# Kernel tuning notes

Measured on AMD Instinct MI355X. Metric: run time of the kernel, lower is better.

Reference implementation:

```python
import jax, jax.numpy as jnp
import numpy as np

B, L, E, H = 2, 2048, 1024, 16
HD = E // H


def _rel_shift(x):
    # x: [b, h, q, k] -> Transformer-XL relative shift via pad+reshape trick
    b, h, q, k = x.shape
    xp = jnp.pad(x, ((0, 0), (0, 0), (0, 0), (1, 0)))  # pad left of last dim
    xp = xp.reshape(b, h, k + 1, q)
    return xp[:, :, 1:, :].reshape(b, h, q, k)


def setup_inputs() -> dict:
    key = jax.random.key(0)
    ks = jax.random.split(key, 16)
    s = 0.02
    return {
        "query": jax.random.normal(ks[0], (B, L, E), jnp.float32),
        "key": jax.random.normal(ks[1], (B, L, E), jnp.float32),
        "value": jax.random.normal(ks[2], (B, L, E), jnp.float32),
        "pos_embedding": jax.random.normal(ks[3], (B, L, E), jnp.float32),
        "Wq": jax.random.normal(ks[4], (E, E), jnp.float32) * s,
        "bq": jnp.zeros((E,), jnp.float32),
        "Wk": jax.random.normal(ks[5], (E, E), jnp.float32) * s,
        "bk": jnp.zeros((E,), jnp.float32),
        "Wv": jax.random.normal(ks[6], (E, E), jnp.float32) * s,
        "bv": jnp.zeros((E,), jnp.float32),
        "Wp": jax.random.normal(ks[7], (E, E), jnp.float32) * s,  # Pos linear, no bias
        "Wo": jax.random.normal(ks[8], (E, E), jnp.float32) * s,
        "bo": jnp.zeros((E,), jnp.float32),
        "U": jax.random.normal(ks[9], (H, HD), jnp.float32) * s,
        "V": jax.random.normal(ks[10], (H, HD), jnp.float32) * s,
    }


def reference(query, key, value, pos_embedding, Wq, bq, Wk, bk, Wv, bv, Wp, Wo, bo, U, V):
    b, qlen, e = query.shape
    h, hd = U.shape
    scale = jnp.sqrt(jnp.asarray(e, query.dtype))
    # torch Linear: y = x @ W.T + b
    q = (query @ Wq.T + bq).reshape(b, qlen, h, hd)
    k = (key @ Wk.T + bk).reshape(b, key.shape[1], h, hd)
    v = (value @ Wv.T + bv).reshape(b, value.shape[1], h, hd)
    r = (pos_embedding @ Wp.T).reshape(b, -1, h, hd)
    content_score = jnp.einsum("bqhd,bkhd->bhqk", q + U, k)
    position_score = jnp.einsum("bqhd,bkhd->bhqk", q + V, r)
    position_score = _rel_shift(position_score)
    attention_score = (content_score + position_score) / scale
    # NOTE: the original module applies NO softmax; faithful reproduction.
    # einsum 'bhqk,bvhd->bqhd' sums over both k (scores) and v (values).
    alpha = jnp.einsum("bhqk,bvhd->bqhd", attention_score, v).reshape(b, qlen, e)
    return alpha @ Wo.T + bo
```

## Files before the change

### kernel.cpp

```cpp
#include <hip/hip_runtime.h>

#define BB 2
#define LL 2048
#define EE 1024
#define HH 16
#define HDD 64

typedef __bf16 bf16x8 __attribute__((ext_vector_type(8)));
typedef float f32x4 __attribute__((ext_vector_type(4)));

__device__ __forceinline__ unsigned short f2bf(float f) {
  unsigned int x = __float_as_uint(f);
  return (unsigned short)((x + 0x7FFFu + ((x >> 16) & 1u)) >> 16);
}

__device__ __forceinline__ float bf2f(unsigned short u) {
  return __uint_as_float((unsigned int)u << 16);
}

__device__ __forceinline__ void load_lds16(const void* g, void* l) {
  __builtin_amdgcn_global_load_lds(
      (const __attribute__((address_space(1))) void*)g,
      (__attribute__((address_space(3))) void*)l, 16, 0, 0);
}

#define SUMKV_BLOCKS 256
#define CAST_BLOCKS 1280
#define CAST_STRIDE (CAST_BLOCKS * 256)
__global__ __launch_bounds__(256) void prelude_kernel(
    const float* __restrict__ q, const float* __restrict__ pe,
    const float* __restrict__ wq, const float* __restrict__ wp,
    unsigned short* __restrict__ q16, unsigned short* __restrict__ pe16,
    unsigned short* __restrict__ wq16, unsigned short* __restrict__ wp16,
    const float* __restrict__ key, const float* __restrict__ value,
    float* __restrict__ keysum, float* __restrict__ valsum) {
  if (blockIdx.x < SUMKV_BLOCKS) {
    int blk2 = blockIdx.x;
    int b = blk2 >> 7, ch = blk2 & 127;
    int tid = threadIdx.x;
    const float4* k4 = (const float4*)(key   + ((size_t)b * LL + ch * 16) * EE);
    const float4* v4 = (const float4*)(value + ((size_t)b * LL + ch * 16) * EE);
    float4 ak = make_float4(0.f, 0.f, 0.f, 0.f);
    float4 av = make_float4(0.f, 0.f, 0.f, 0.f);
#pragma unroll 8
    for (int i = 0; i < 16; i++) {
      float4 kk = k4[i * 256 + tid];
      float4 vv = v4[i * 256 + tid];
      ak.x += kk.x; ak.y += kk.y; ak.z += kk.z; ak.w += kk.w;
      av.x += vv.x; av.y += vv.y; av.z += vv.z; av.w += vv.w;
    }
    int e = tid * 4;
    atomicAdd(&keysum[b * EE + e + 0], ak.x);
    atomicAdd(&keysum[b * EE + e + 1], ak.y);
    atomicAdd(&keysum[b * EE + e + 2], ak.z);
    atomicAdd(&keysum[b * EE + e + 3], ak.w);
    atomicAdd(&valsum[b * EE + e + 0], av.x);
    atomicAdd(&valsum[b * EE + e + 1], av.y);
    atomicAdd(&valsum[b * EE + e + 2], av.z);
    atomicAdd(&valsum[b * EE + e + 3], av.w);
  } else {
    const int NQ4 = BB * LL * EE / 4;
    const int NW4 = EE * EE / 4;
    int t = (blockIdx.x - SUMKV_BLOCKS) * 256 + threadIdx.x;
    float4 v[8]; unsigned short* dst[8]; int off[8];
#pragma unroll
    for (int k = 0; k < 8; k++) {
      int i = t + k * CAST_STRIDE;
      const float* src;
      if (i < NQ4)                { src = q;  dst[k] = q16;  off[k] = i; }
      else if (i < 2 * NQ4)       { src = pe; dst[k] = pe16; off[k] = i - NQ4; }
      else if (i < 2 * NQ4 + NW4) { src = wq; dst[k] = wq16; off[k] = i - 2 * NQ4; }
      else                        { src = wp; dst[k] = wp16; off[k] = i - 2 * NQ4 - NW4; }
      v[k] = ((const float4*)src)[off[k]];
    }
#pragma unroll
    for (int k = 0; k < 8; k++) {
      ushort4 u;
      u.x = f2bf(v[k].x); u.y = f2bf(v[k].y); u.z = f2bf(v[k].z); u.w = f2bf(v[k].w);
      ((ushort4*)dst[k])[off[k]] = u;
    }
  }
}

__global__ __launch_bounds__(256) void proj_kernel(
    const float* __restrict__ keysum, const float* __restrict__ valsum,
    const float* __restrict__ Wk, const float* __restrict__ bk,
    const float* __restrict__ Wv, const float* __restrict__ bv,
    float* __restrict__ Kproj, float* __restrict__ Vproj) {
  int wv = threadIdx.x >> 6, lane = threadIdx.x & 63;
  int idx = blockIdx.x * 4 + wv;
  int b = idx >> 10, ep = idx & (EE - 1);
  const float* sum  = blockIdx.z ? valsum : keysum;
  const float* W    = blockIdx.z ? Wv : Wk;
  const float* bias = blockIdx.z ? bv : bk;
  float* outp       = blockIdx.z ? Vproj : Kproj;
  float acc = 0.f;
  for (int k = lane; k < EE; k += 64) acc += sum[b * EE + k] * W[ep * EE + k];
  for (int off = 32; off; off >>= 1) acc += __shfl_down(acc, off, 64);
  if (lane == 0) outp[b * EE + ep] = acc + (float)LL * bias[ep];
}

__global__ __launch_bounds__(256) void gemm_kernel(
    const unsigned short* __restrict__ q16, const unsigned short* __restrict__ wq16,
    const float* __restrict__ bq, unsigned short* __restrict__ qout,
    const unsigned short* __restrict__ pe16, const unsigned short* __restrict__ wp16,
    unsigned short* __restrict__ rout, float* __restrict__ chunks,
    const float* __restrict__ Vproj, const float* __restrict__ Wo,
    float* __restrict__ W2) {
  const int tid = threadIdx.x;
  const int lane = tid & 63;
  const int wv = tid >> 6;

  if (blockIdx.z == 2) {
    int bid = blockIdx.x + 32 * blockIdx.y;
    int wslot = bid * 4 + wv;
    int base = wslot * 32;
    int b = base >> 14;
    int h = (base >> 10) & (HH - 1);
    int e0 = base & (EE - 1);
    float vp = Vproj[b * EE + h * HDD + lane];
    const float* wo = Wo + (size_t)e0 * EE + h * HDD + lane;
    for (int r = 0; r < 32; r++) {
      float acc = vp * wo[(size_t)r * EE];
      for (int off = 32; off; off >>= 1) acc += __shfl_down(acc, off, 64);
      if (lane == 0) W2[((size_t)b * HH + h) * EE + e0 + r] = acc;
    }
    return;
  }

  const int K = EE, N = EE;
  const unsigned short* X; const unsigned short* W; const float* bias;
  unsigned short* Out;
  if (blockIdx.z == 0) { X = q16;  W = wq16; bias = bq;      Out = qout; }
  else                 { X = pe16; W = wp16; bias = nullptr; Out = rout; }

  __shared__ __align__(16) unsigned short As[2][128 * 32];
  __shared__ __align__(16) unsigned short Bs[2][128 * 32];

  const int wr = wv >> 1, wc = wv & 1;
  const int m0 = blockIdx.x * 128;
  const int n0 = blockIdx.y * 128;

  const int srow = wv * 16 + (lane >> 2);
  const int s_src = ((lane & 3) - ((lane >> 3) & 3)) & 3;
  const unsigned short* gA = X + (size_t)(m0 + srow) * K + s_src * 8;
  const unsigned short* gB = W + (size_t)(n0 + srow) * K + s_src * 8;

  f32x4 acc[4][4];
#pragma unroll
  for (int i = 0; i < 4; i++)
#pragma unroll
    for (int j = 0; j < 4; j++) acc[i][j] = (f32x4)0.0f;

  const int arow = wr * 64 + (lane & 15);
  const int brow = wc * 64 + (lane & 15);
  const int koff = (((lane >> 4) + ((lane & 15) >> 1)) & 3) * 8;

#define GSTAGE(BI, KK)                                                   \
  do {                                                                   \
    load_lds16(gA + (KK),                  &As[BI][wv * 512]);           \
    load_lds16(gA + (KK) + (size_t)64 * K, &As[BI][wv * 512 + 2048]);    \
    load_lds16(gB + (KK),                  &Bs[BI][wv * 512]);           \
    load_lds16(gB + (KK) + (size_t)64 * K, &Bs[BI][wv * 512 + 2048]);    \
  } while (0)

  GSTAGE(0, 0);
  __syncthreads();
  int bi = 0;
  for (int t = 0; t < K / 32; ++t) {
    if (t + 1 < K / 32) GSTAGE(bi ^ 1, (t + 1) * 32);
    bf16x8 af[4], bf[4];
#pragma unroll
    for (int i = 0; i < 4; i++)
      af[i] = *(const bf16x8*)&As[bi][(arow + i * 16) * 32 + koff];
#pragma unroll
    for (int j = 0; j < 4; j++)
      bf[j] = *(const bf16x8*)&Bs[bi][(brow + j * 16) * 32 + koff];
#pragma unroll
    for (int i = 0; i < 4; i++)
#pragma unroll
      for (int j = 0; j < 4; j++)
        acc[i][j] = __builtin_amdgcn_mfma_f32_16x16x32_bf16(af[i], bf[j], acc[i][j], 0, 0, 0);
    __syncthreads();
    bi ^= 1;
  }
#undef GSTAGE

  const int rbase = m0 + wr * 64 + (lane >> 4) * 4;
  const int cbase = n0 + wc * 64 + (lane & 15);
#pragma unroll
  for (int i = 0; i < 4; i++) {
#pragma unroll
    for (int j = 0; j < 4; j++) {
      int col = cbase + j * 16;
      float badd = bias ? bias[col] : 0.f;
#pragma unroll
      for (int g = 0; g < 4; g++) {
        int row = rbase + i * 16 + g;
        Out[(size_t)row * N + col] = f2bf(acc[i][j][g] + badd);
      }
    }
  }

  if (blockIdx.z == 1) {
    int b = m0 >> 11;
    int ch0 = ((m0 & (LL - 1)) >> 5) + wr * 2;
#pragma unroll
    for (int cp = 0; cp < 2; cp++) {
#pragma unroll
      for (int j = 0; j < 4; j++) {
        float s = 0.f;
#pragma unroll
        for (int i = cp * 2; i < cp * 2 + 2; i++)
#pragma unroll
          for (int g = 0; g < 4; g++) s += acc[i][j][g];
        s += __shfl_down(s, 32, 64);
        s += __shfl_down(s, 16, 64);
        if (lane < 16) {
          int col = n0 + wc * 64 + j * 16 + lane;
          chunks[((size_t)b * 64 + ch0 + cp) * EE + col] = s;
        }
      }
    }
  }
}

__global__ __launch_bounds__(256) void scan2f_kernel(
    const unsigned short* __restrict__ qbuf, const unsigned short* __restrict__ rbuf,
    const float* __restrict__ chunks, const float* __restrict__ Kproj,
    const float* __restrict__ U, const float* __restrict__ V,
    float* __restrict__ S1, float* __restrict__ Dbuf) {
  int tid = threadIdx.x, lane = tid & 63;
  int hg = blockIdx.x, ch = blockIdx.y, b = blockIdx.z;
  int e = hg * 256 + tid;
  int h = hg * 4 + (tid >> 6);
  float pre = 0.f, tot = 0.f;
  for (int c = 0; c < 64; c++) {
    float cs = chunks[((size_t)b * 64 + c) * EE + e];
    tot += cs;
    if (c < ch) pre += cs;
  }
  float kp = Kproj[b * EE + e], Ue = U[e], Ve = V[e];
  float run = pre;
  size_t hoff = ((size_t)b * HH + h) * LL;
#pragma unroll 4
  for (int i = 0; i < 32; i++) {
    int m = ch * 32 + i;
    int p = LL - 1 - m;
    float qv = bf2f(qbuf[((size_t)b * LL + p) * EE + e]);
    float rv = bf2f(rbuf[((size_t)b * LL + m) * EE + e]);
    float tq = qv + Ve;
    float d = tq * run;
    float s = tq * tot + (qv + Ue) * kp;
#pragma unroll
    for (int off = 32; off; off >>= 1) {
      d += __shfl_down(d, off, 64);
      s += __shfl_down(s, off, 64);
    }
    if (lane == 0) { Dbuf[hoff + m] = d; S1[hoff + p] = s; }
    run += rv;
  }
}

__global__ __launch_bounds__(256) void out_kernel(
    const float* __restrict__ S1, const float* __restrict__ Dbuf,
    const float* __restrict__ W2, const float* __restrict__ bo,
    float* __restrict__ out) {
  int row0 = blockIdx.x * 8;
  int b = row0 >> 11, p0 = row0 & (LL - 1);
  int tid = threadIdx.x;
  __shared__ float sh[8][HH];
  if (tid < 128) {
    int rr = tid >> 4, h = tid & 15;
    int p = p0 + rr;
    size_t hoff = ((size_t)b * HH + h) * LL;
    float s1 = S1[hoff + p];
    float d1 = Dbuf[hoff + (LL - 1 - p)];
    float d2 = (p == LL - 1) ? 0.f : Dbuf[hoff + (LL - 2 - p)];
    sh[rr][h] = (s1 - d1 + d2) * (1.f / 32.f);
  }
  float4 w2r[HH];
#pragma unroll
  for (int h = 0; h < HH; h++)
    w2r[h] = ((const float4*)(W2 + ((size_t)b * HH + h) * EE))[tid];
  float4 bo4 = ((const float4*)bo)[tid];
  __syncthreads();
#pragma unroll
  for (int rr = 0; rr < 8; rr++) {
    float4 acc = bo4;
#pragma unroll
    for (int h = 0; h < HH; h++) {
      float s = sh[rr][h];
      acc.x += s * w2r[h].x; acc.y += s * w2r[h].y;
      acc.z += s * w2r[h].z; acc.w += s * w2r[h].w;
    }
    ((float4*)out)[(size_t)(row0 + rr) * 256 + tid] = acc;
  }
}

extern "C" void kernel_launch(void* const* d_in, const int* in_sizes, int n_in,
                              void* d_out, int out_size, void* d_ws, size_t ws_size,
                              hipStream_t stream) {
  const float* query = (const float*)d_in[0];
  const float* key   = (const float*)d_in[1];
  const float* value = (const float*)d_in[2];
  const float* pos   = (const float*)d_in[3];
  const float* Wq = (const float*)d_in[4];
  const float* bq = (const float*)d_in[5];
  const float* Wk = (const float*)d_in[6];
  const float* bk = (const float*)d_in[7];
  const float* Wv = (const float*)d_in[8];
  const float* bv = (const float*)d_in[9];
  const float* Wp = (const float*)d_in[10];
  const float* Wo = (const float*)d_in[11];
  const float* bo = (const float*)d_in[12];
  const float* U  = (const float*)d_in[13];
  const float* V  = (const float*)d_in[14];
  float* out = (float*)d_out;

  char* ws = (char*)d_ws;
  size_t o = 0;
  auto take = [&](size_t bytes) -> char* {
    char* p = ws + o;
    o += (bytes + 255) & ~(size_t)255;
    return p;
  };
  float* keysum = (float*)take(BB * EE * 4);
  float* valsum = (float*)take(BB * EE * 4);
  float* Kproj  = (float*)take(BB * EE * 4);
  float* Vproj  = (float*)take(BB * EE * 4);
  float* W2     = (float*)take((size_t)BB * HH * EE * 4);
  float* S1     = (float*)take((size_t)BB * HH * LL * 4);
  float* Dbuf   = (float*)take((size_t)BB * HH * LL * 4);
  float* chunks = (float*)take((size_t)BB * 64 * EE * 4);
  unsigned short* qbuf = (unsigned short*)take((size_t)BB * LL * EE * 2);
  unsigned short* rbuf = (unsigned short*)take((size_t)BB * LL * EE * 2);
  unsigned short* q16  = (unsigned short*)take((size_t)BB * LL * EE * 2);
  unsigned short* pe16 = (unsigned short*)take((size_t)BB * LL * EE * 2);
  unsigned short* wq16 = (unsigned short*)take((size_t)EE * EE * 2);
  unsigned short* wp16 = (unsigned short*)take((size_t)EE * EE * 2);

  hipMemsetAsync(keysum, 0, (size_t)2 * BB * EE * 4, stream);

  prelude_kernel<<<SUMKV_BLOCKS + CAST_BLOCKS, 256, 0, stream>>>(
      query, pos, Wq, Wp, q16, pe16, wq16, wp16, key, value, keysum, valsum);
  proj_kernel<<<dim3(BB * EE / 4, 1, 2), 256, 0, stream>>>(
      keysum, valsum, Wk, bk, Wv, bv, Kproj, Vproj);
  gemm_kernel<<<dim3(BB * LL / 128, EE / 128, 3), 256, 0, stream>>>(
      q16, wq16, bq, qbuf, pe16, wp16, rbuf, chunks, Vproj, Wo, W2);
  scan2f_kernel<<<dim3(4, 64, BB), 256, 0, stream>>>(qbuf, rbuf, chunks, Kproj, U, V, S1, Dbuf);
  out_kernel<<<dim3(BB * LL / 8), 256, 0, stream>>>(S1, Dbuf, W2, bo, out);
}
```

Measured before the change: 226.5 us.

## Halve GEMM N-tile to 64 and split scan into 16-row chunks

The projection GEMM tile changes from 128x128 to 128x64, which doubles the block count so more CUs stay busy, and adds a launch-bounds occupancy hint. The fused pos-projection chunk sums now cover 16 rows instead of 32, so the scan kernel launches twice as many blocks, each handling 16 rows. Surplus z=2 blocks exit early. The trade-off is lower MFMA reuse per block, more redundant A-tile loads, and a longer prefix loop over 128 chunks in the scan.

```diff
diff --git a/kernel.cpp b/kernel.cpp
--- a/kernel.cpp
+++ b/kernel.cpp
@@ -100,7 +100,7 @@
   if (lane == 0) outp[b * EE + ep] = acc + (float)LL * bias[ep];
 }
 
-__global__ __launch_bounds__(256) void gemm_kernel(
+__global__ __launch_bounds__(256, 5) void gemm_kernel(
     const unsigned short* __restrict__ q16, const unsigned short* __restrict__ wq16,
     const float* __restrict__ bq, unsigned short* __restrict__ qout,
     const unsigned short* __restrict__ pe16, const unsigned short* __restrict__ wp16,
@@ -113,6 +113,7 @@
 
   if (blockIdx.z == 2) {
     int bid = blockIdx.x + 32 * blockIdx.y;
+    if (bid >= 256) return;
     int wslot = bid * 4 + wv;
     int base = wslot * 32;
     int b = base >> 14;
@@ -135,33 +136,33 @@
   else                 { X = pe16; W = wp16; bias = nullptr; Out = rout; }
 
   __shared__ __align__(16) unsigned short As[2][128 * 32];
-  __shared__ __align__(16) unsigned short Bs[2][128 * 32];
-
-  const int wr = wv >> 1, wc = wv & 1;
+  __shared__ __align__(16) unsigned short Bs[2][64 * 32];
+
+  const int wm = wv >> 1, wn = wv & 1;
   const int m0 = blockIdx.x * 128;
-  const int n0 = blockIdx.y * 128;
-
-  const int srow = wv * 16 + (lane >> 2);
+  const int n0 = blockIdx.y * 64;
+
+  const int srow_a = wv * 32 + (lane >> 2);
+  const int srow_b = wv * 16 + (lane >> 2);
   const int s_src = ((lane & 3) - ((lane >> 3) & 3)) & 3;
-  const unsigned short* gA = X + (size_t)(m0 + srow) * K + s_src * 8;
-  const unsigned short* gB = W + (size_t)(n0 + srow) * K + s_src * 8;
-
-  f32x4 acc[4][4];
+  const unsigned short* gA = X + (size_t)(m0 + srow_a) * K + s_src * 8;
+  const unsigned short* gB = W + (size_t)(n0 + srow_b) * K + s_src * 8;
+
+  f32x4 acc[4][2];
 #pragma unroll
   for (int i = 0; i < 4; i++)
 #pragma unroll
-    for (int j = 0; j < 4; j++) acc[i][j] = (f32x4)0.0f;
-
-  const int arow = wr * 64 + (lane & 15);
-  const int brow = wc * 64 + (lane & 15);
+    for (int j = 0; j < 2; j++) acc[i][j] = (f32x4)0.0f;
+
+  const int arow = wm * 64 + (lane & 15);
+  const int brow = wn * 32 + (lane & 15);
   const int koff = (((lane >> 4) + ((lane & 15) >> 1)) & 3) * 8;
 
-#define GSTAGE(BI, KK)                                                   \
-  do {                                                                   \
-    load_lds16(gA + (KK),                  &As[BI][wv * 512]);           \
-    load_lds16(gA + (KK) + (size_t)64 * K, &As[BI][wv * 512 + 2048]);    \
-    load_lds16(gB + (KK),                  &Bs[BI][wv * 512]);           \
-    load_lds16(gB + (KK) + (size_t)64 * K, &Bs[BI][wv * 512 + 2048]);    \
+#define GSTAGE(BI, KK)                                                    \
+  do {                                                                    \
+    load_lds16(gA + (KK),                  &As[BI][wv * 1024]);           \
+    load_lds16(gA + (KK) + (size_t)16 * K, &As[BI][wv * 1024 + 512]);     \
+    load_lds16(gB + (KK),                  &Bs[BI][wv * 512]);            \
   } while (0)
 
   GSTAGE(0, 0);
@@ -169,29 +170,29 @@
   int bi = 0;
   for (int t = 0; t < K / 32; ++t) {
     if (t + 1 < K / 32) GSTAGE(bi ^ 1, (t + 1) * 32);
-    bf16x8 af[4], bf[4];
+    bf16x8 af[4], bf[2];
 #pragma unroll
     for (int i = 0; i < 4; i++)
       af[i] = *(const bf16x8*)&As[bi][(arow + i * 16) * 32 + koff];
 #pragma unroll
-    for (int j = 0; j < 4; j++)
+    for (int j = 0; j < 2; j++)
       bf[j] = *(const bf16x8*)&Bs[bi][(brow + j * 16) * 32 + koff];
 #pragma unroll
     for (int i = 0; i < 4; i++)
 #pragma unroll
-      for (int j = 0; j < 4; j++)
+      for (int j = 0; j < 2; j++)
         acc[i][j] = __builtin_amdgcn_mfma_f32_16x16x32_bf16(af[i], bf[j], acc[i][j], 0, 0, 0);
     __syncthreads();
     bi ^= 1;
   }
 #undef GSTAGE
 
-  const int rbase = m0 + wr * 64 + (lane >> 4) * 4;
-  const int cbase = n0 + wc * 64 + (lane & 15);
+  const int rbase = m0 + wm * 64 + (lane >> 4) * 4;
+  const int cbase = n0 + wn * 32 + (lane & 15);
 #pragma unroll
   for (int i = 0; i < 4; i++) {
 #pragma unroll
-    for (int j = 0; j < 4; j++) {
+    for (int j = 0; j < 2; j++) {
       int col = cbase + j * 16;
       float badd = bias ? bias[col] : 0.f;
 #pragma unroll
@@ -204,21 +205,17 @@
 
   if (blockIdx.z == 1) {
     int b = m0 >> 11;
-    int ch0 = ((m0 & (LL - 1)) >> 5) + wr * 2;
-#pragma unroll
-    for (int cp = 0; cp < 2; cp++) {
-#pragma unroll
-      for (int j = 0; j < 4; j++) {
-        float s = 0.f;
-#pragma unroll
-        for (int i = cp * 2; i < cp * 2 + 2; i++)
-#pragma unroll
-          for (int g = 0; g < 4; g++) s += acc[i][j][g];
+    int ch0 = ((m0 & (LL - 1)) >> 4) + wm * 4;
+#pragma unroll
+    for (int i = 0; i < 4; i++) {
+#pragma unroll
+      for (int j = 0; j < 2; j++) {
+        float s = acc[i][j][0] + acc[i][j][1] + acc[i][j][2] + acc[i][j][3];
         s += __shfl_down(s, 32, 64);
         s += __shfl_down(s, 16, 64);
         if (lane < 16) {
-          int col = n0 + wc * 64 + j * 16 + lane;
-          chunks[((size_t)b * 64 + ch0 + cp) * EE + col] = s;
+          int col = n0 + wn * 32 + j * 16 + lane;
+          chunks[((size_t)b * 128 + ch0 + i) * EE + col] = s;
         }
       }
     }
@@ -235,8 +232,8 @@
   int e = hg * 256 + tid;
   int h = hg * 4 + (tid >> 6);
   float pre = 0.f, tot = 0.f;
-  for (int c = 0; c < 64; c++) {
-    float cs = chunks[((size_t)b * 64 + c) * EE + e];
+  for (int c = 0; c < 128; c++) {
+    float cs = chunks[((size_t)b * 128 + c) * EE + e];
     tot += cs;
     if (c < ch) pre += cs;
   }
@@ -244,8 +241,8 @@
   float run = pre;
   size_t hoff = ((size_t)b * HH + h) * LL;
 #pragma unroll 4
-  for (int i = 0; i < 32; i++) {
-    int m = ch * 32 + i;
+  for (int i = 0; i < 16; i++) {
+    int m = ch * 16 + i;
     int p = LL - 1 - m;
     float qv = bf2f(qbuf[((size_t)b * LL + p) * EE + e]);
     float rv = bf2f(rbuf[((size_t)b * LL + m) * EE + e]);
@@ -332,7 +329,7 @@
   float* W2     = (float*)take((size_t)BB * HH * EE * 4);
   float* S1     = (float*)take((size_t)BB * HH * LL * 4);
   float* Dbuf   = (float*)take((size_t)BB * HH * LL * 4);
-  float* chunks = (float*)take((size_t)BB * 64 * EE * 4);
+  float* chunks = (float*)take((size_t)BB * 128 * EE * 4);
   unsigned short* qbuf = (unsigned short*)take((size_t)BB * LL * EE * 2);
   unsigned short* rbuf = (unsigned short*)take((size_t)BB * LL * EE * 2);
   unsigned short* q16  = (unsigned short*)take((size_t)BB * LL * EE * 2);
@@ -346,8 +343,8 @@
       query, pos, Wq, Wp, q16, pe16, wq16, wp16, key, value, keysum, valsum);
   proj_kernel<<<dim3(BB * EE / 4, 1, 2), 256, 0, stream>>>(
       keysum, valsum, Wk, bk, Wv, bv, Kproj, Vproj);
-  gemm_kernel<<<dim3(BB * LL / 128, EE / 128, 3), 256, 0, stream>>>(
+  gemm_kernel<<<dim3(BB * LL / 128, EE / 64, 3), 256, 0, stream>>>(
       q16, wq16, bq, qbuf, pe16, wp16, rbuf, chunks, Vproj, Wo, W2);
-  scan2f_kernel<<<dim3(4, 64, BB), 256, 0, stream>>>(qbuf, rbuf, chunks, Kproj, U, V, S1, Dbuf);
+  scan2f_kernel<<<dim3(4, 128, BB), 256, 0, stream>>>(qbuf, rbuf, chunks, Kproj, U, V, S1, Dbuf);
   out_kernel<<<dim3(BB * LL / 8), 256, 0, stream>>>(S1, Dbuf, W2, bo, out);
 }
```

Result: faster. 219.2 us (-3.2%).
